# Kernel optimization log

Measured on AMD Instinct MI355X. Metric: run time of the kernel, lower is better.

Reference implementation:

```python
import jax, jax.numpy as jnp
import numpy as np

N = 100000
IN_C, HID_C, OUT_C = 128, 128, 64
E = 1600000


def setup_inputs() -> dict:
    key = jax.random.key(0)
    ks = jax.random.split(key, 8)
    x = jax.random.normal(ks[0], (N, IN_C), dtype=jnp.float32)
    edge_index = jax.random.randint(ks[1], (2, E), 0, N, dtype=jnp.int64)
    def glorot(k, fan_in, fan_out):
        lim = np.sqrt(6.0 / (fan_in + fan_out)).astype(np.float32)
        return jax.random.uniform(k, (fan_in, fan_out), jnp.float32, -lim, lim)
    return {
        "x": x,
        "edge_index": edge_index,
        "W1l": glorot(ks[2], IN_C, HID_C),   # lin_l: aggregated neighbors
        "W1r": glorot(ks[3], IN_C, HID_C),   # lin_r: root/self
        "b1": jnp.zeros((HID_C,), jnp.float32),
        "W2l": glorot(ks[4], HID_C, OUT_C),
        "W2r": glorot(ks[5], HID_C, OUT_C),
        "b2": jnp.zeros((OUT_C,), jnp.float32),
    }


def _sage_conv(x, src, dst, Wl, Wr, b):
    # mean aggregation over incoming edges: gather source feats, segment-sum at dst
    msg_sum = jax.ops.segment_sum(x[src], dst, num_segments=N)          # [N, C_in]
    deg = jax.ops.segment_sum(jnp.ones((src.shape[0],), x.dtype), dst,
                              num_segments=N)                           # [N]
    mean = msg_sum / jnp.clip(deg, 1.0, None)[:, None]
    return mean @ Wl + x @ Wr + b


def reference(x, edge_index, W1l, W1r, b1, W2l, W2r, b2):
    src, dst = edge_index[0], edge_index[1]
    h = jax.nn.relu(_sage_conv(x, src, dst, W1l, W1r, b1))
    out = _sage_conv(h, src, dst, W2l, W2r, b2)
    return out
```

## Files before the change

kernel.cpp:

```cpp
#include <hip/hip_runtime.h>
#include <type_traits>


constexpr int K = 128;
constexpr int EB = 4096;

typedef __bf16 bf16x2 __attribute__((ext_vector_type(2)));
typedef __bf16 bf16x4 __attribute__((ext_vector_type(4)));
typedef __bf16 bf16x8 __attribute__((ext_vector_type(8)));
typedef float f32x4 __attribute__((ext_vector_type(4)));
typedef float f32x2 __attribute__((ext_vector_type(2)));


__device__ __forceinline__ unsigned char to_fp8(float v) {
#if __has_builtin(__builtin_amdgcn_cvt_pk_fp8_f32)
  int p = __builtin_amdgcn_cvt_pk_fp8_f32(v, v, 0, false);
  return (unsigned char)(p & 0xff);
#else
  unsigned u = __builtin_bit_cast(unsigned, v);
  unsigned s = (u >> 24) & 0x80u;
  float a = fabsf(v);
  if (a > 448.f) a = 448.f;
  unsigned bits;
  if (a < 0.015625f) {
    bits = (unsigned)(a * 512.f + 0.5f);
  } else {
    unsigned b = __builtin_bit_cast(unsigned, a);
    b += ((b >> 20) & 1) + 0x0007FFFF;
    unsigned e = (b >> 23) - 120;
    bits = (e << 3) | ((b >> 20) & 7);
    if (bits > 0x7E) bits = 0x7E;
  }
  return (unsigned char)(s | bits);
#endif
}

__device__ __forceinline__ f32x2 from_fp8x2(unsigned short u) {
#if __has_builtin(__builtin_amdgcn_cvt_pk_f32_fp8)
  return __builtin_amdgcn_cvt_pk_f32_fp8((int)u, false);
#else
  f32x2 r;
  unsigned b0 = u & 0xff, b1 = (u >> 8) & 0xff;
  unsigned e0 = (b0 >> 3) & 15, m0 = b0 & 7;
  unsigned e1 = (b1 >> 3) & 15, m1 = b1 & 7;
  float v0 = e0 ? __builtin_bit_cast(float, ((e0 + 120) << 23) | (m0 << 20))
              : (float)m0 * 0.001953125f;
  float v1 = e1 ? __builtin_bit_cast(float, ((e1 + 120) << 23) | (m1 << 20))
              : (float)m1 * 0.001953125f;
  r[0] = (b0 & 0x80) ? -v0 : v0;
  r[1] = (b1 & 0x80) ? -v1 : v1;
  return r;
#endif
}

__device__ __forceinline__ f32x2 fp8x2_lo(unsigned v) {
#if __has_builtin(__builtin_amdgcn_cvt_pk_f32_fp8)
  return __builtin_amdgcn_cvt_pk_f32_fp8((int)v, false);
#else
  return from_fp8x2((unsigned short)(v & 0xffffu));
#endif
}

__device__ __forceinline__ f32x2 fp8x2_hi(unsigned v) {
#if __has_builtin(__builtin_amdgcn_cvt_pk_f32_fp8)
  return __builtin_amdgcn_cvt_pk_f32_fp8((int)v, true);
#else
  return from_fp8x2((unsigned short)(v >> 16));
#endif
}


template <int COLS>
__global__ __launch_bounds__(256) void k_wprep(const float* __restrict__ W,
                                               __bf16* __restrict__ Bt) {
  int idx = blockIdx.x * 256 + threadIdx.x;
  int k = idx / COLS, c = idx % COLS;
  Bt[c * K + k] = (__bf16)W[idx];
}


__global__ __launch_bounds__(256) void k_bhist(const int* __restrict__ dst,
                                               int* __restrict__ blockHist,
                                               int* __restrict__ bucketTotal,
                                               int E, int n, int nB) {
  extern __shared__ int hist[];
  for (int i = threadIdx.x; i < nB; i += 256) hist[i] = 0;
  __syncthreads();
  int base = blockIdx.x * EB, end = min(base + EB, E);
  for (int e = base + threadIdx.x; e < end; e += 256) {
    int d = dst[e];
    if ((unsigned)d < (unsigned)n) atomicAdd(&hist[d >> 8], 1);
  }
  __syncthreads();
  for (int i = threadIdx.x; i < nB; i += 256) {
    int v = hist[i];
    blockHist[(long)blockIdx.x * nB + i] = v;
    if (v) atomicAdd(&bucketTotal[i], v);
  }
}

__global__ __launch_bounds__(512) void k_btop(const int* __restrict__ bucketTotal,
                                              int* __restrict__ bucketBase,
                                              int* __restrict__ bucketCursor, int nB) {
  __shared__ int sh[512];
  int t = threadIdx.x;
  int s = (t < nB) ? bucketTotal[t] : 0;
  sh[t] = s;
  __syncthreads();
  for (int off = 1; off < 512; off <<= 1) {
    int v = (t >= off) ? sh[t - off] : 0;
    __syncthreads();
    sh[t] += v;
    __syncthreads();
  }
  if (t < nB) {
    int base = sh[t] - s;
    bucketBase[t] = base;
    bucketCursor[t] = base;
    if (t == nB - 1) bucketBase[nB] = sh[t];
  }
}

__global__ __launch_bounds__(256) void k_bscatter(const int* __restrict__ src,
                                                  const int* __restrict__ dst,
                                                  const int* __restrict__ blockHist,
                                                  int* __restrict__ bucketCursor,
                                                  unsigned* __restrict__ recs,
                                                  int E, int n, int nB) {
  extern __shared__ int cur[];
  for (int i = threadIdx.x; i < nB; i += 256) {
    int c = blockHist[(long)blockIdx.x * nB + i];
    cur[i] = c ? atomicAdd(&bucketCursor[i], c) : 0;
  }
  __syncthreads();
  int base = blockIdx.x * EB, end = min(base + EB, E);
  for (int e = base + threadIdx.x; e < end; e += 256) {
    int d = dst[e];
    if ((unsigned)d < (unsigned)n) {
      int s = min(max(src[e], 0), n - 1);
      int pos = atomicAdd(&cur[d >> 8], 1);
      recs[pos] = ((unsigned)s << 8) | (unsigned)(d & 255);
    }
  }
}

__global__ __launch_bounds__(256) void k_bfill(const unsigned* __restrict__ recs,
                                               const int* __restrict__ bucketBase,
                                               int* __restrict__ rowptr,
                                               int* __restrict__ col, int n, int nB) {
  __shared__ int degl[256];
  __shared__ int incl[256];
  int b = blockIdx.x, t = threadIdx.x;
  int rbeg = bucketBase[b], rend = bucketBase[b + 1];
  degl[t] = 0;
  __syncthreads();
  for (int i = rbeg + t; i < rend; i += 256)
    atomicAdd(&degl[recs[i] & 255], 1);
  __syncthreads();
  incl[t] = degl[t];
  __syncthreads();
  for (int off = 1; off < 256; off <<= 1) {
    int v = (t >= off) ? incl[t - off] : 0;
    __syncthreads();
    incl[t] += v;
    __syncthreads();
  }
  int excl = incl[t] - degl[t];
  int node = b * 256 + t;
  if (node <= n) rowptr[node] = rbeg + excl;
  __syncthreads();
  degl[t] = rbeg + excl;
  __syncthreads();
  for (int i = rbeg + t; i < rend; i += 256) {
    unsigned r = recs[i];
    int pos = atomicAdd(&degl[r & 255], 1);
    col[pos] = (int)(r >> 8);
  }
}


template <int COLS, typename TIN>
__global__ __launch_bounds__(256) void k_gemm_mfma(const TIN* __restrict__ X,
                                                   const __bf16* __restrict__ Bta,
                                                   const __bf16* __restrict__ Btb,
                                                   unsigned char* __restrict__ outA,
                                                   __bf16* __restrict__ outB, int nrows) {
  constexpr int LD = 136;
  constexpr int MT_N = COLS / 32;
  __shared__ __bf16 sh[(64 + COLS) * LD];
  __bf16* As = sh;
  __bf16* Bt = sh + 64 * LD;

  bool isA = (blockIdx.y == 0);
  const __bf16* Btg = isA ? Bta : Btb;

  int tid = threadIdx.x;
  long row0 = (long)blockIdx.x * 64;

  if constexpr (std::is_same_v<TIN, float>) {
#pragma unroll
    for (int it = 0; it < 8; ++it) {
      int i = tid + it * 256;
      int r = i >> 5, c4 = (i & 31) << 2;
      long row = row0 + r;
      float4 v = make_float4(0.f, 0.f, 0.f, 0.f);
      if (row < nrows) v = *(const float4*)(X + row * K + c4);
      bf16x4 bb;
      bb[0] = (__bf16)v.x; bb[1] = (__bf16)v.y; bb[2] = (__bf16)v.z; bb[3] = (__bf16)v.w;
      *(bf16x4*)&As[r * LD + c4] = bb;
    }
  } else {
#pragma unroll
    for (int it = 0; it < 4; ++it) {
      int i = tid + it * 256;
      int r = i >> 4, c8 = (i & 15) << 3;
      long row = row0 + r;
      bf16x8 v = {};
      if (row < nrows) v = *(const bf16x8*)(X + row * K + c8);
      *(bf16x8*)&As[r * LD + c8] = v;
    }
  }
#pragma unroll
  for (int it = 0; it < (COLS * 16) / 256; ++it) {
    int i = tid + it * 256;
    int c = i >> 4, kk = (i & 15) << 3;
    *(bf16x8*)&Bt[c * LD + kk] = *(const bf16x8*)(Btg + c * K + kk);
  }
  __syncthreads();

  int w = tid >> 6, lane = tid & 63;
  int m = lane & 15, quad = lane >> 4;
  int wrow = (w >> 1) * 32;
  int wcol = (w & 1) * (COLS / 2);

  f32x4 acc[2][MT_N];
#pragma unroll
  for (int mi = 0; mi < 2; ++mi)
#pragma unroll
    for (int ni = 0; ni < MT_N; ++ni) acc[mi][ni] = (f32x4){0.f, 0.f, 0.f, 0.f};

#pragma unroll
  for (int kc = 0; kc < 4; ++kc) {
    int ko = kc * 32 + quad * 8;
    bf16x8 af[2];
#pragma unroll
    for (int mi = 0; mi < 2; ++mi)
      af[mi] = *(const bf16x8*)&As[(wrow + mi * 16 + m) * LD + ko];
    bf16x8 bfr[MT_N];
#pragma unroll
    for (int ni = 0; ni < MT_N; ++ni)
      bfr[ni] = *(const bf16x8*)&Bt[(wcol + ni * 16 + m) * LD + ko];
#pragma unroll
    for (int mi = 0; mi < 2; ++mi)
#pragma unroll
      for (int ni = 0; ni < MT_N; ++ni)
        acc[mi][ni] = __builtin_amdgcn_mfma_f32_16x16x32_bf16(af[mi], bfr[ni], acc[mi][ni], 0, 0, 0);
  }

#pragma unroll
  for (int mi = 0; mi < 2; ++mi) {
#pragma unroll
    for (int r = 0; r < 4; ++r) {
      long grow = row0 + wrow + mi * 16 + quad * 4 + r;
      if (grow < nrows) {
#pragma unroll
        for (int ni = 0; ni < MT_N; ++ni) {
          long idx = grow * COLS + wcol + ni * 16 + m;
          float v = acc[mi][ni][r];
          if (isA) outA[idx] = to_fp8(v);
          else     outB[idx] = (__bf16)v;
        }
      }
    }
  }
}


template <bool RELU>
__global__ __launch_bounds__(256) void k_agg128(const unsigned char* __restrict__ Y,
                                                const __bf16* __restrict__ XR,
                                                const float* __restrict__ bias,
                                                const int* __restrict__ rowptr,
                                                const int* __restrict__ col,
                                                __bf16* __restrict__ out, int nnodes) {
  int wave = threadIdx.x >> 6, lane = threadIdx.x & 63;
  int quarter = lane >> 4, l = lane & 15;
  int sb = lane & 48;
  int n = blockIdx.x * 16 + wave * 4 + quarter;
  bool valid = n < nnodes;
  int beg = 0, end = 0;
  if (valid) {
    beg = rowptr[n];
    end = rowptr[n + 1];
  }
  int co = l * 8;
  const unsigned char* Yc = Y + co;

  f32x2 av0 = {0.f, 0.f}, av1 = {0.f, 0.f}, av2 = {0.f, 0.f}, av3 = {0.f, 0.f};

  for (int base = beg; base < end; base += 16) {
    int cnt = min(end - base, 16);
    int idx = (l < cnt) ? col[base + l] : 0;
    int j = 0;
    for (; j + 3 < cnt; j += 4) {
      long s0 = (unsigned)__shfl(idx, sb + j);
      long s1 = (unsigned)__shfl(idx, sb + j + 1);
      long s2 = (unsigned)__shfl(idx, sb + j + 2);
      long s3 = (unsigned)__shfl(idx, sb + j + 3);
      uint2 v0 = *(const uint2*)(Yc + s0 * 128);
      uint2 v1 = *(const uint2*)(Yc + s1 * 128);
      uint2 v2 = *(const uint2*)(Yc + s2 * 128);
      uint2 v3 = *(const uint2*)(Yc + s3 * 128);
      av0 += fp8x2_lo(v0.x); av1 += fp8x2_hi(v0.x);
      av2 += fp8x2_lo(v0.y); av3 += fp8x2_hi(v0.y);
      av0 += fp8x2_lo(v1.x); av1 += fp8x2_hi(v1.x);
      av2 += fp8x2_lo(v1.y); av3 += fp8x2_hi(v1.y);
      av0 += fp8x2_lo(v2.x); av1 += fp8x2_hi(v2.x);
      av2 += fp8x2_lo(v2.y); av3 += fp8x2_hi(v2.y);
      av0 += fp8x2_lo(v3.x); av1 += fp8x2_hi(v3.x);
      av2 += fp8x2_lo(v3.y); av3 += fp8x2_hi(v3.y);
    }
    for (; j < cnt; ++j) {
      long s = (unsigned)__shfl(idx, sb + j);
      uint2 v = *(const uint2*)(Yc + s * 128);
      av0 += fp8x2_lo(v.x); av1 += fp8x2_hi(v.x);
      av2 += fp8x2_lo(v.y); av3 += fp8x2_hi(v.y);
    }
  }

  if (valid) {
    float inv = 1.f / (float)max(end - beg, 1);
    bf16x8 xv = *(const bf16x8*)(XR + (long)n * 128 + co);
    f32x4 b0 = *(const f32x4*)(bias + co);
    f32x4 b1 = *(const f32x4*)(bias + co + 4);
    float r0 = av0[0] * inv + (float)xv[0] + b0[0];
    float r1 = av0[1] * inv + (float)xv[1] + b0[1];
    float r2 = av1[0] * inv + (float)xv[2] + b0[2];
    float r3 = av1[1] * inv + (float)xv[3] + b0[3];
    float r4 = av2[0] * inv + (float)xv[4] + b1[0];
    float r5 = av2[1] * inv + (float)xv[5] + b1[1];
    float r6 = av3[0] * inv + (float)xv[6] + b1[2];
    float r7 = av3[1] * inv + (float)xv[7] + b1[3];
    if (RELU) {
      r0 = fmaxf(r0, 0.f); r1 = fmaxf(r1, 0.f);
      r2 = fmaxf(r2, 0.f); r3 = fmaxf(r3, 0.f);
      r4 = fmaxf(r4, 0.f); r5 = fmaxf(r5, 0.f);
      r6 = fmaxf(r6, 0.f); r7 = fmaxf(r7, 0.f);
    }
    bf16x8 o;
    o[0] = (__bf16)r0; o[1] = (__bf16)r1; o[2] = (__bf16)r2; o[3] = (__bf16)r3;
    o[4] = (__bf16)r4; o[5] = (__bf16)r5; o[6] = (__bf16)r6; o[7] = (__bf16)r7;
    *(bf16x8*)(out + (long)n * 128 + co) = o;
  }
}

__global__ __launch_bounds__(256) void k_agg64(const unsigned char* __restrict__ Y,
                                               const __bf16* __restrict__ XR,
                                               const float* __restrict__ bias,
                                               const int* __restrict__ rowptr,
                                               const int* __restrict__ col,
                                               float* __restrict__ out, int nnodes) {
  int wave = threadIdx.x >> 6, lane = threadIdx.x & 63;
  int quarter = lane >> 4, l = lane & 15;
  int sb = lane & 48;
  int n = blockIdx.x * 16 + wave * 4 + quarter;
  bool valid = n < nnodes;
  int beg = 0, end = 0;
  if (valid) {
    beg = rowptr[n];
    end = rowptr[n + 1];
  }
  int co = l * 4;
  const unsigned char* Yc = Y + co;

  f32x2 av0 = {0.f, 0.f}, av1 = {0.f, 0.f};

  for (int base = beg; base < end; base += 16) {
    int cnt = min(end - base, 16);
    int idx = (l < cnt) ? col[base + l] : 0;
    int j = 0;
    for (; j + 3 < cnt; j += 4) {
      long s0 = (unsigned)__shfl(idx, sb + j);
      long s1 = (unsigned)__shfl(idx, sb + j + 1);
      long s2 = (unsigned)__shfl(idx, sb + j + 2);
      long s3 = (unsigned)__shfl(idx, sb + j + 3);
      unsigned v0 = *(const unsigned*)(Yc + s0 * 64);
      unsigned v1 = *(const unsigned*)(Yc + s1 * 64);
      unsigned v2 = *(const unsigned*)(Yc + s2 * 64);
      unsigned v3 = *(const unsigned*)(Yc + s3 * 64);
      av0 += fp8x2_lo(v0); av1 += fp8x2_hi(v0);
      av0 += fp8x2_lo(v1); av1 += fp8x2_hi(v1);
      av0 += fp8x2_lo(v2); av1 += fp8x2_hi(v2);
      av0 += fp8x2_lo(v3); av1 += fp8x2_hi(v3);
    }
    for (; j < cnt; ++j) {
      long s = (unsigned)__shfl(idx, sb + j);
      unsigned v = *(const unsigned*)(Yc + s * 64);
      av0 += fp8x2_lo(v); av1 += fp8x2_hi(v);
    }
  }

  if (valid) {
    float inv = 1.f / (float)max(end - beg, 1);
    bf16x4 xv = *(const bf16x4*)(XR + (long)n * 64 + co);
    f32x4 bv = *(const f32x4*)(bias + co);
    f32x4 r;
    r[0] = av0[0] * inv + (float)xv[0] + bv[0];
    r[1] = av0[1] * inv + (float)xv[1] + bv[1];
    r[2] = av1[0] * inv + (float)xv[2] + bv[2];
    r[3] = av1[1] * inv + (float)xv[3] + bv[3];
    *(f32x4*)(out + (long)n * 64 + co) = r;
  }
}


extern "C" void kernel_launch(void* const* d_in, const int* in_sizes, int n_in,
                              void* d_out, int out_size, void* d_ws, size_t ws_size,
                              hipStream_t stream) {
  const float* x   = (const float*)d_in[0];
  const int*   ei  = (const int*)d_in[1];
  const float* W1l = (const float*)d_in[2];
  const float* W1r = (const float*)d_in[3];
  const float* b1  = (const float*)d_in[4];
  const float* W2l = (const float*)d_in[5];
  const float* W2r = (const float*)d_in[6];
  const float* b2  = (const float*)d_in[7];
  float* out = (float*)d_out;

  int N = in_sizes[0] / K;
  int E = in_sizes[1] / 2;
  const int* src = ei;
  const int* dst = ei + E;

  int nB = (N + 255) >> 8;
  int nblk = (E + EB - 1) / EB;

  char* ws = (char*)d_ws;
  size_t off = 0;
  auto alloc = [&](size_t bytes) {
    void* p = ws + off;
    off = (off + bytes + 255) & ~(size_t)255;
    return p;
  };
  int*      rowptr       = (int*)alloc(((size_t)N + 2) * 4);
  int*      col          = (int*)alloc((size_t)E * 4);
  int*      blockHist    = (int*)alloc((size_t)nblk * nB * 4);
  int*      bucketTotal  = (int*)alloc(((size_t)nB) * 4);
  int*      bucketBase   = (int*)alloc(((size_t)nB + 1) * 4);
  int*      bucketCursor = (int*)alloc((size_t)nB * 4);
  unsigned* recs         = (unsigned*)alloc((size_t)E * 4);
  unsigned char* y1      = (unsigned char*)alloc((size_t)N * 128);
  __bf16*   xr           = (__bf16*)alloc((size_t)N * 128 * 2);
  __bf16*   h            = (__bf16*)alloc((size_t)N * 128 * 2);
  __bf16*   Bt1l         = (__bf16*)alloc((size_t)128 * K * 2);
  __bf16*   Bt1r         = (__bf16*)alloc((size_t)128 * K * 2);
  __bf16*   Bt2l         = (__bf16*)alloc((size_t)64 * K * 2);
  __bf16*   Bt2r         = (__bf16*)alloc((size_t)64 * K * 2);
  unsigned char* y2 = y1;
  __bf16*   hr = xr;

  k_wprep<128><<<(K * 128) / 256, 256, 0, stream>>>(W1l, Bt1l);
  k_wprep<128><<<(K * 128) / 256, 256, 0, stream>>>(W1r, Bt1r);
  k_wprep<64><<<(K * 64) / 256, 256, 0, stream>>>(W2l, Bt2l);
  k_wprep<64><<<(K * 64) / 256, 256, 0, stream>>>(W2r, Bt2r);

  hipMemsetAsync(bucketTotal, 0, (size_t)nB * 4, stream);
  k_bhist<<<nblk, 256, nB * 4, stream>>>(dst, blockHist, bucketTotal, E, N, nB);
  k_btop<<<1, 512, 0, stream>>>(bucketTotal, bucketBase, bucketCursor, nB);
  k_bscatter<<<nblk, 256, nB * 4, stream>>>(src, dst, blockHist, bucketCursor, recs, E, N, nB);
  k_bfill<<<nB, 256, 0, stream>>>(recs, bucketBase, rowptr, col, N, nB);

  int gx = (N + 63) / 64;
  k_gemm_mfma<128, float><<<dim3(gx, 2), 256, 0, stream>>>(x, Bt1l, Bt1r, y1, xr, N);
  k_agg128<true><<<(N + 15) / 16, 256, 0, stream>>>(y1, xr, b1, rowptr, col, h, N);

  k_gemm_mfma<64, __bf16><<<dim3(gx, 2), 256, 0, stream>>>(h, Bt2l, Bt2r, y2, hr, N);
  k_agg64<<<(N + 15) / 16, 256, 0, stream>>>(y2, hr, b2, rowptr, col, out, N);
}
```

Measured before the change: 279.3 us.

## Fuse both weight GEMMs per row tile and merge weight-prep launches

The GEMM kernel now handles both the neighbor (lin_l) and root (lin_r) weight matrices in one block, so the input row tile is loaded and converted to bf16 once instead of twice. B fragments are read directly from global memory (L2-resident) instead of being staged in shared memory, which cuts LDS usage and the staging sync. The four weight-prep launches are merged into one kernel. The trade-off is uncoalesced global B loads inside the MFMA loop and half as many blocks per GEMM.

```diff
diff --git a/kernel.cpp b/kernel.cpp
--- a/kernel.cpp
+++ b/kernel.cpp
@@ -70,11 +70,27 @@
 }
 
 
-template <int COLS>
-__global__ __launch_bounds__(256) void k_wprep(const float* __restrict__ W,
-                                               __bf16* __restrict__ Bt) {
-  int idx = blockIdx.x * 256 + threadIdx.x;
-  int k = idx / COLS, c = idx % COLS;
+__global__ __launch_bounds__(256) void k_wprep_all(
+    const float* __restrict__ W1l, const float* __restrict__ W1r,
+    const float* __restrict__ W2l, const float* __restrict__ W2r,
+    __bf16* __restrict__ B1l, __bf16* __restrict__ B1r,
+    __bf16* __restrict__ B2l, __bf16* __restrict__ B2r) {
+  int b = blockIdx.x;
+  const float* W;
+  __bf16* Bt;
+  int idx;
+  bool wide;
+  if (b < 64) {
+    W = W1l; Bt = B1l; idx = b * 256 + threadIdx.x; wide = true;
+  } else if (b < 128) {
+    W = W1r; Bt = B1r; idx = (b - 64) * 256 + threadIdx.x; wide = true;
+  } else if (b < 160) {
+    W = W2l; Bt = B2l; idx = (b - 128) * 256 + threadIdx.x; wide = false;
+  } else {
+    W = W2r; Bt = B2r; idx = (b - 160) * 256 + threadIdx.x; wide = false;
+  }
+  int k = wide ? (idx >> 7) : (idx >> 6);
+  int c = wide ? (idx & 127) : (idx & 63);
   Bt[c * K + k] = (__bf16)W[idx];
 }
 
@@ -180,19 +196,14 @@
 
 
 template <int COLS, typename TIN>
-__global__ __launch_bounds__(256) void k_gemm_mfma(const TIN* __restrict__ X,
-                                                   const __bf16* __restrict__ Bta,
-                                                   const __bf16* __restrict__ Btb,
-                                                   unsigned char* __restrict__ outA,
-                                                   __bf16* __restrict__ outB, int nrows) {
+__global__ __launch_bounds__(256) void k_gemm_fused(const TIN* __restrict__ X,
+                                                    const __bf16* __restrict__ Bta,
+                                                    const __bf16* __restrict__ Btb,
+                                                    unsigned char* __restrict__ outA,
+                                                    __bf16* __restrict__ outB, int nrows) {
   constexpr int LD = 136;
   constexpr int MT_N = COLS / 32;
-  __shared__ __bf16 sh[(64 + COLS) * LD];
-  __bf16* As = sh;
-  __bf16* Bt = sh + 64 * LD;
-
-  bool isA = (blockIdx.y == 0);
-  const __bf16* Btg = isA ? Bta : Btb;
+  __shared__ __bf16 As[64 * LD];
 
   int tid = threadIdx.x;
   long row0 = (long)blockIdx.x * 64;
@@ -220,12 +231,6 @@
       *(bf16x8*)&As[r * LD + c8] = v;
     }
   }
-#pragma unroll
-  for (int it = 0; it < (COLS * 16) / 256; ++it) {
-    int i = tid + it * 256;
-    int c = i >> 4, kk = (i & 15) << 3;
-    *(bf16x8*)&Bt[c * LD + kk] = *(const bf16x8*)(Btg + c * K + kk);
-  }
   __syncthreads();
 
   int w = tid >> 6, lane = tid & 63;
@@ -233,42 +238,47 @@
   int wrow = (w >> 1) * 32;
   int wcol = (w & 1) * (COLS / 2);
 
-  f32x4 acc[2][MT_N];
-#pragma unroll
-  for (int mi = 0; mi < 2; ++mi)
-#pragma unroll
-    for (int ni = 0; ni < MT_N; ++ni) acc[mi][ni] = (f32x4){0.f, 0.f, 0.f, 0.f};
-
-#pragma unroll
-  for (int kc = 0; kc < 4; ++kc) {
-    int ko = kc * 32 + quad * 8;
-    bf16x8 af[2];
+#pragma unroll
+  for (int p = 0; p < 2; ++p) {
+    const __bf16* Btg = p ? Btb : Bta;
+
+    f32x4 acc[2][MT_N];
 #pragma unroll
     for (int mi = 0; mi < 2; ++mi)
-      af[mi] = *(const bf16x8*)&As[(wrow + mi * 16 + m) * LD + ko];
-    bf16x8 bfr[MT_N];
-#pragma unroll
-    for (int ni = 0; ni < MT_N; ++ni)
-      bfr[ni] = *(const bf16x8*)&Bt[(wcol + ni * 16 + m) * LD + ko];
-#pragma unroll
-    for (int mi = 0; mi < 2; ++mi)
+#pragma unroll
+      for (int ni = 0; ni < MT_N; ++ni) acc[mi][ni] = (f32x4){0.f, 0.f, 0.f, 0.f};
+
+#pragma unroll
+    for (int kc = 0; kc < 4; ++kc) {
+      int ko = kc * 32 + quad * 8;
+      bf16x8 af[2];
+#pragma unroll
+      for (int mi = 0; mi < 2; ++mi)
+        af[mi] = *(const bf16x8*)&As[(wrow + mi * 16 + m) * LD + ko];
+      bf16x8 bfr[MT_N];
 #pragma unroll
       for (int ni = 0; ni < MT_N; ++ni)
-        acc[mi][ni] = __builtin_amdgcn_mfma_f32_16x16x32_bf16(af[mi], bfr[ni], acc[mi][ni], 0, 0, 0);
-  }
-
-#pragma unroll
-  for (int mi = 0; mi < 2; ++mi) {
-#pragma unroll
-    for (int r = 0; r < 4; ++r) {
-      long grow = row0 + wrow + mi * 16 + quad * 4 + r;
-      if (grow < nrows) {
-#pragma unroll
-        for (int ni = 0; ni < MT_N; ++ni) {
-          long idx = grow * COLS + wcol + ni * 16 + m;
-          float v = acc[mi][ni][r];
-          if (isA) outA[idx] = to_fp8(v);
-          else     outB[idx] = (__bf16)v;
+        bfr[ni] = *(const bf16x8*)(Btg + (long)(wcol + ni * 16 + m) * K + ko);
+#pragma unroll
+      for (int mi = 0; mi < 2; ++mi)
+#pragma unroll
+        for (int ni = 0; ni < MT_N; ++ni)
+          acc[mi][ni] = __builtin_amdgcn_mfma_f32_16x16x32_bf16(af[mi], bfr[ni], acc[mi][ni], 0, 0, 0);
+    }
+
+#pragma unroll
+    for (int mi = 0; mi < 2; ++mi) {
+#pragma unroll
+      for (int r = 0; r < 4; ++r) {
+        long grow = row0 + wrow + mi * 16 + quad * 4 + r;
+        if (grow < nrows) {
+#pragma unroll
+          for (int ni = 0; ni < MT_N; ++ni) {
+            long idx = grow * COLS + wcol + ni * 16 + m;
+            float v = acc[mi][ni][r];
+            if (p == 0) outA[idx] = to_fp8(v);
+            else        outB[idx] = (__bf16)v;
+          }
         }
       }
     }
@@ -459,10 +469,7 @@
   unsigned char* y2 = y1;
   __bf16*   hr = xr;
 
-  k_wprep<128><<<(K * 128) / 256, 256, 0, stream>>>(W1l, Bt1l);
-  k_wprep<128><<<(K * 128) / 256, 256, 0, stream>>>(W1r, Bt1r);
-  k_wprep<64><<<(K * 64) / 256, 256, 0, stream>>>(W2l, Bt2l);
-  k_wprep<64><<<(K * 64) / 256, 256, 0, stream>>>(W2r, Bt2r);
+  k_wprep_all<<<192, 256, 0, stream>>>(W1l, W1r, W2l, W2r, Bt1l, Bt1r, Bt2l, Bt2r);
 
   hipMemsetAsync(bucketTotal, 0, (size_t)nB * 4, stream);
   k_bhist<<<nblk, 256, nB * 4, stream>>>(dst, blockHist, bucketTotal, E, N, nB);
@@ -471,9 +478,9 @@
   k_bfill<<<nB, 256, 0, stream>>>(recs, bucketBase, rowptr, col, N, nB);
 
   int gx = (N + 63) / 64;
-  k_gemm_mfma<128, float><<<dim3(gx, 2), 256, 0, stream>>>(x, Bt1l, Bt1r, y1, xr, N);
+  k_gemm_fused<128, float><<<gx, 256, 0, stream>>>(x, Bt1l, Bt1r, y1, xr, N);
   k_agg128<true><<<(N + 15) / 16, 256, 0, stream>>>(y1, xr, b1, rowptr, col, h, N);
 
-  k_gemm_mfma<64, __bf16><<<dim3(gx, 2), 256, 0, stream>>>(h, Bt2l, Bt2r, y2, hr, N);
+  k_gemm_fused<64, __bf16><<<gx, 256, 0, stream>>>(h, Bt2l, Bt2r, y2, hr, N);
   k_agg64<<<(N + 15) / 16, 256, 0, stream>>>(y2, hr, b2, rowptr, col, out, N);
 }
```

Result: slower. 288.0 us (+3.1%).
